# Performance work log

Measured on AMD Instinct MI355X. Metric: run time of the kernel, lower is better.

Reference implementation:

```python
import jax, jax.numpy as jnp
import numpy as np

B, T, IN, H, OUT = 512, 2048, 16, 128, 8


def setup_inputs() -> dict:
    key = jax.random.key(0)
    ks = jax.random.split(key, 12)
    s = 0.05
    return {
        "x": jax.random.normal(ks[0], (B, T, IN), dtype=jnp.float32),
        "W_ih0": jax.random.normal(ks[1], (3 * H, IN), dtype=jnp.float32) * s,
        "W_hh0": jax.random.normal(ks[2], (3 * H, H), dtype=jnp.float32) * s,
        "b_ih0": jax.random.normal(ks[3], (3 * H,), dtype=jnp.float32) * s,
        "b_hh0": jax.random.normal(ks[4], (3 * H,), dtype=jnp.float32) * s,
        "W_ih1": jax.random.normal(ks[5], (3 * H, H), dtype=jnp.float32) * s,
        "W_hh1": jax.random.normal(ks[6], (3 * H, H), dtype=jnp.float32) * s,
        "b_ih1": jax.random.normal(ks[7], (3 * H,), dtype=jnp.float32) * s,
        "b_hh1": jax.random.normal(ks[8], (3 * H,), dtype=jnp.float32) * s,
        "W_out": jax.random.normal(ks[9], (OUT, H), dtype=jnp.float32) * s,
        "b_out": jax.random.normal(ks[10], (OUT,), dtype=jnp.float32) * s,
    }


def _gru_cell(xg, h, W_hh, b_hh):
    # xg: precomputed x @ W_ih.T + b_ih, shape [B, 3H]; PyTorch gate order r,z,n
    hg = h @ W_hh.T + b_hh
    xr, xz, xn = jnp.split(xg, 3, axis=-1)
    hr, hz, hn = jnp.split(hg, 3, axis=-1)
    r = jax.nn.sigmoid(xr + hr)
    z = jax.nn.sigmoid(xz + hz)
    n = jnp.tanh(xn + r * hn)
    return (1.0 - z) * n + z * h


def reference(x, W_ih0, W_hh0, b_ih0, b_hh0, W_ih1, W_hh1, b_ih1, b_hh1, W_out, b_out):
    # Precompute layer-0 input gates for all timesteps: [T, B, 3H]
    xg0 = jnp.einsum('bti,gi->tbg', x, W_ih0) + b_ih0

    def step(carry, xg_t):
        h0, h1 = carry
        h0 = _gru_cell(xg_t, h0, W_hh0, b_hh0)
        xg1 = h0 @ W_ih1.T + b_ih1
        h1 = _gru_cell(xg1, h1, W_hh1, b_hh1)
        return (h0, h1), h1

    h0 = jnp.zeros((x.shape[0], W_hh0.shape[1]), dtype=x.dtype)
    h1 = jnp.zeros((x.shape[0], W_hh1.shape[1]), dtype=x.dtype)
    _, h1_seq = jax.lax.scan(step, (h0, h1), xg0)  # [T, B, H]
    out = jnp.einsum('tbh,oh->bto', h1_seq, W_out) + b_out  # [B, T, OUT]
    return out
```

## Files before the change

kernel.cpp:

```cpp
#include <hip/hip_runtime.h>


typedef unsigned int  uint;
typedef unsigned short ushort;
typedef _Float16 v8h __attribute__((ext_vector_type(8)));
typedef float    v4f __attribute__((ext_vector_type(4)));
typedef uint     v2u __attribute__((ext_vector_type(2)));

#define Tq   2048
#define INq  16
#define Hq   128
#define OUTq 8
#define BW   16

#define MFMA(a,b,c) __builtin_amdgcn_mfma_f32_16x16x32_f16((a),(b),(c),0,0,0)
#define BAR() do { asm volatile("s_waitcnt lgkmcnt(0)" ::: "memory"); \
                   __builtin_amdgcn_s_barrier(); \
                   asm volatile("" ::: "memory"); } while(0)

__device__ __forceinline__ float sigm(float x){
  return __builtin_amdgcn_rcpf(1.0f + __expf(-x));
}
__device__ __forceinline__ float tanh_f(float x){
  return 1.0f - 2.0f*__builtin_amdgcn_rcpf(__expf(2.0f*x) + 1.0f);
}
__device__ __forceinline__ uint packh2(float lo, float hi){
  _Float16 a=(_Float16)lo, b=(_Float16)hi;
  return (uint)__builtin_bit_cast(ushort,a) | ((uint)__builtin_bit_cast(ushort,b)<<16);
}
__device__ __forceinline__ v4f ld4(const float* p){
  return *reinterpret_cast<const v4f*>(p);
}

__global__ __launch_bounds__(512,2) void gru2_kernel(
    const float* __restrict__ x,
    const float* __restrict__ Wih0, const float* __restrict__ Whh0,
    const float* __restrict__ bih0, const float* __restrict__ bhh0,
    const float* __restrict__ Wih1, const float* __restrict__ Whh1,
    const float* __restrict__ bih1, const float* __restrict__ bhh1,
    const float* __restrict__ Wout, const float* __restrict__ bout,
    float* __restrict__ out)
{
  const int tid  = threadIdx.x;
  const int lane = tid & 63;
  const int w    = tid >> 6;
  const int nb   = lane & 15;
  const int bg   = lane >> 4;
  const int b0   = blockIdx.x * BW;
  const int hb   = 16*w + nb;

  __shared__ __align__(16) _Float16 hA0[2][2048];
  __shared__ __align__(16) _Float16 hA1[2][2048];
  for (int i=tid; i<2048; i+=512){ ((uint*)hA0)[i]=0u; ((uint*)hA1)[i]=0u; }

  const float* xrow = x + (size_t)(b0+nb)*Tq*INq;
  float4 xfa, xfb;
  if (bg < 2){
    xfa = *(const float4*)(xrow + 0*INq + bg*8);
    xfb = *(const float4*)(xrow + 0*INq + bg*8 + 4);
  }

  v8h Fhh0[3][4], Fih1[3][4], Fhh1[3][4], Fx[3], Fo[4];
  #pragma unroll
  for (int g=0; g<3; ++g){
    const int r = g*Hq + hb;
    #pragma unroll
    for (int ks=0; ks<4; ++ks){
      const float* p0 = &Whh0[r*Hq + ks*32 + bg*8];
      const float* p1 = &Wih1[r*Hq + ks*32 + bg*8];
      const float* p2 = &Whh1[r*Hq + ks*32 + bg*8];
      v8h a, b, c;
      #pragma unroll
      for (int e=0;e<8;++e){ a[e]=(_Float16)p0[e]; b[e]=(_Float16)p1[e]; c[e]=(_Float16)p2[e]; }
      Fhh0[g][ks]=a; Fih1[g][ks]=b; Fhh1[g][ks]=c;
    }
    v8h vx;
    #pragma unroll
    for (int e=0;e<8;++e) vx[e]=(_Float16)0.f;
    if (bg < 2){
      const float* p = &Wih0[r*INq + bg*8];
      #pragma unroll
      for (int e=0;e<8;++e) vx[e]=(_Float16)p[e];
    }
    Fx[g]=vx;
  }
  #pragma unroll
  for (int ks=0; ks<4; ++ks){
    v8h v;
    #pragma unroll
    for (int e=0;e<8;++e) v[e]=(_Float16)0.f;
    if (nb < OUTq){
      const float* p = &Wout[nb*Hq + ks*32 + bg*8];
      #pragma unroll
      for (int e=0;e<8;++e) v[e]=(_Float16)p[e];
    }
    Fo[ks]=v;
  }

  const int hb4 = 16*w + bg*4;
  const v4f bR4  = ld4(bih0+hb4)      + ld4(bhh0+hb4);
  const v4f bZ4  = ld4(bih0+Hq+hb4)   + ld4(bhh0+Hq+hb4);
  const v4f bNX4 = ld4(bih0+2*Hq+hb4);
  const v4f bNH4 = ld4(bhh0+2*Hq+hb4);
  const v4f cR4  = ld4(bih1+hb4)      + ld4(bhh1+hb4);
  const v4f cZ4  = ld4(bih1+Hq+hb4)   + ld4(bhh1+Hq+hb4);
  const v4f cNX4 = ld4(bih1+2*Hq+hb4);
  const v4f cNH4 = ld4(bhh1+2*Hq+hb4);
  v4f bo4 = {0.f,0.f,0.f,0.f};
  if (bg < 2) bo4 = ld4(bout + bg*4);

  float h0s[4] = {0,0,0,0};
  float h1s[4] = {0,0,0,0};

  int rb[4];
  #pragma unroll
  for (int ks=0; ks<4; ++ks) rb[ks] = nb*128 + (((ks*4+bg) ^ nb))*8;
  const int wof = nb*128 + (((2*w + (bg>>1)) ^ nb))*8 + (bg&1)*4;

  __syncthreads();

  for (int t=0; t<Tq; ++t){
    const int cur = t&1, prv = cur^1;

    v8h ax;
    #pragma unroll
    for (int e=0;e<8;++e) ax[e]=(_Float16)0.f;
    if (bg < 2){
      ax[0]=(_Float16)xfa.x; ax[1]=(_Float16)xfa.y; ax[2]=(_Float16)xfa.z; ax[3]=(_Float16)xfa.w;
      ax[4]=(_Float16)xfb.x; ax[5]=(_Float16)xfb.y; ax[6]=(_Float16)xfb.z; ax[7]=(_Float16)xfb.w;
    }

    v4f aR=bR4, aZ=bZ4, aNX=bNX4, aNH=bNH4;
    aR  = MFMA(Fx[0], ax, aR);
    aZ  = MFMA(Fx[1], ax, aZ);
    aNX = MFMA(Fx[2], ax, aNX);
    if (bg < 2){
      const int tn = (t+1 < Tq) ? t+1 : Tq-1;
      xfa = *(const float4*)(xrow + tn*INq + bg*8);
      xfb = *(const float4*)(xrow + tn*INq + bg*8 + 4);
    }
    #pragma unroll
    for (int ks=0; ks<4; ++ks){
      v8h a = *(const v8h*)&hA0[prv][rb[ks]];
      aR  = MFMA(Fhh0[0][ks], a, aR);
      aZ  = MFMA(Fhh0[1][ks], a, aZ);
      aNH = MFMA(Fhh0[2][ks], a, aNH);
    }
    float hn0[4];
    #pragma unroll
    for (int j=0;j<4;++j){
      float r = sigm(aR[j]);
      float z = sigm(aZ[j]);
      float n = tanh_f(aNX[j] + r*aNH[j]);
      float h = n + z*(h0s[j]-n);
      h0s[j]=h; hn0[j]=h;
    }
    { v2u pk; pk[0]=packh2(hn0[0],hn0[1]); pk[1]=packh2(hn0[2],hn0[3]);
      *(v2u*)&hA0[cur][wof] = pk; }
    BAR();

    v4f cR=cR4, cZ=cZ4, cNX=cNX4, cNH=cNH4;
    #pragma unroll
    for (int ks=0; ks<4; ++ks){
      v8h a0 = *(const v8h*)&hA0[cur][rb[ks]];
      v8h a1 = *(const v8h*)&hA1[prv][rb[ks]];
      cR  = MFMA(Fih1[0][ks], a0, cR);
      cZ  = MFMA(Fih1[1][ks], a0, cZ);
      cNX = MFMA(Fih1[2][ks], a0, cNX);
      cR  = MFMA(Fhh1[0][ks], a1, cR);
      cZ  = MFMA(Fhh1[1][ks], a1, cZ);
      cNH = MFMA(Fhh1[2][ks], a1, cNH);
    }
    if (w == 7){
      v4f oac = {0.f,0.f,0.f,0.f};
      #pragma unroll
      for (int ks=0; ks<4; ++ks){
        v8h a1 = *(const v8h*)&hA1[prv][rb[ks]];
        oac = MFMA(Fo[ks], a1, oac);
      }
      if (t > 0 && bg < 2){
        float4 o;
        o.x=oac[0]+bo4[0]; o.y=oac[1]+bo4[1]; o.z=oac[2]+bo4[2]; o.w=oac[3]+bo4[3];
        *(float4*)&out[((size_t)(b0+nb)*Tq + (t-1))*OUTq + bg*4] = o;
      }
    }
    float hn1[4];
    #pragma unroll
    for (int j=0;j<4;++j){
      float r = sigm(cR[j]);
      float z = sigm(cZ[j]);
      float n = tanh_f(cNX[j] + r*cNH[j]);
      float h = n + z*(h1s[j]-n);
      h1s[j]=h; hn1[j]=h;
    }
    { v2u pk; pk[0]=packh2(hn1[0],hn1[1]); pk[1]=packh2(hn1[2],hn1[3]);
      *(v2u*)&hA1[cur][wof] = pk; }
    BAR();
  }

  if (w == 7){
    v4f oac = {0.f,0.f,0.f,0.f};
    #pragma unroll
    for (int ks=0; ks<4; ++ks){
      v8h a1 = *(const v8h*)&hA1[1][rb[ks]];
      oac = MFMA(Fo[ks], a1, oac);
    }
    if (bg < 2){
      float4 o;
      o.x=oac[0]+bo4[0]; o.y=oac[1]+bo4[1]; o.z=oac[2]+bo4[2]; o.w=oac[3]+bo4[3];
      *(float4*)&out[((size_t)(b0+nb)*Tq + (Tq-1))*OUTq + bg*4] = o;
    }
  }
}

extern "C" void kernel_launch(void* const* d_in, const int* in_sizes, int n_in,
                              void* d_out, int out_size, void* d_ws, size_t ws_size,
                              hipStream_t stream) {
  const float* x    = (const float*)d_in[0];
  const float* Wih0 = (const float*)d_in[1];
  const float* Whh0 = (const float*)d_in[2];
  const float* bih0 = (const float*)d_in[3];
  const float* bhh0 = (const float*)d_in[4];
  const float* Wih1 = (const float*)d_in[5];
  const float* Whh1 = (const float*)d_in[6];
  const float* bih1 = (const float*)d_in[7];
  const float* bhh1 = (const float*)d_in[8];
  const float* Wout = (const float*)d_in[9];
  const float* bo   = (const float*)d_in[10];
  gru2_kernel<<<dim3(32), dim3(512), 0, stream>>>(
      x, Wih0, Whh0, bih0, bhh0, Wih1, Whh1, bih1, bhh1, Wout, bo,
      (float*)d_out);
}
```

Baseline: 3.296 ms.

## Skew layer-1 by one timestep to use one barrier per step

Restructures the recurrence so that each tick computes layer 0 for step t and layer 1 for step t-1 together, both reading only state from the previous tick. This halves the block-wide barriers per timestep and lets the MFMA chains for the two layers interleave. Biases move to shared memory to free registers, and the x prefetch is deepened to two steps with a manual unroll by two. The cost is an extra drain tick and more complex buffer indexing, plus possible register pressure from holding both layers' fragments at once.

```diff
diff --git a/kernel.cpp b/kernel.cpp
--- a/kernel.cpp
+++ b/kernel.cpp
@@ -27,9 +27,6 @@
 __device__ __forceinline__ uint packh2(float lo, float hi){
   _Float16 a=(_Float16)lo, b=(_Float16)hi;
   return (uint)__builtin_bit_cast(ushort,a) | ((uint)__builtin_bit_cast(ushort,b)<<16);
-}
-__device__ __forceinline__ v4f ld4(const float* p){
-  return *reinterpret_cast<const v4f*>(p);
 }
 
 __global__ __launch_bounds__(512,2) void gru2_kernel(
@@ -48,16 +45,32 @@
   const int bg   = lane >> 4;
   const int b0   = blockIdx.x * BW;
   const int hb   = 16*w + nb;
+  const int hb4  = 16*w + bg*4;
 
   __shared__ __align__(16) _Float16 hA0[2][2048];
   __shared__ __align__(16) _Float16 hA1[2][2048];
+  __shared__ __align__(16) float    bl[1024];
   for (int i=tid; i<2048; i+=512){ ((uint*)hA0)[i]=0u; ((uint*)hA1)[i]=0u; }
+  for (int i=tid; i<1024; i+=512){
+    const int k=i>>7, h=i&127; float v;
+    if      (k==0) v = bih0[h]       + bhh0[h];
+    else if (k==1) v = bih0[128+h]   + bhh0[128+h];
+    else if (k==2) v = bih0[256+h];
+    else if (k==3) v = bhh0[256+h];
+    else if (k==4) v = bih1[h]       + bhh1[h];
+    else if (k==5) v = bih1[128+h]   + bhh1[128+h];
+    else if (k==6) v = bih1[256+h];
+    else           v = bhh1[256+h];
+    bl[i]=v;
+  }
 
   const float* xrow = x + (size_t)(b0+nb)*Tq*INq;
-  float4 xfa, xfb;
+  float4 xqa[2], xqb[2];
   if (bg < 2){
-    xfa = *(const float4*)(xrow + 0*INq + bg*8);
-    xfb = *(const float4*)(xrow + 0*INq + bg*8 + 4);
+    xqa[0]=*(const float4*)(xrow + 0*INq + bg*8);
+    xqb[0]=*(const float4*)(xrow + 0*INq + bg*8 + 4);
+    xqa[1]=*(const float4*)(xrow + 1*INq + bg*8);
+    xqb[1]=*(const float4*)(xrow + 1*INq + bg*8 + 4);
   }
 
   v8h Fhh0[3][4], Fih1[3][4], Fhh1[3][4], Fx[3], Fo[4];
@@ -96,107 +109,114 @@
     }
     Fo[ks]=v;
   }
-
-  const int hb4 = 16*w + bg*4;
-  const v4f bR4  = ld4(bih0+hb4)      + ld4(bhh0+hb4);
-  const v4f bZ4  = ld4(bih0+Hq+hb4)   + ld4(bhh0+Hq+hb4);
-  const v4f bNX4 = ld4(bih0+2*Hq+hb4);
-  const v4f bNH4 = ld4(bhh0+2*Hq+hb4);
-  const v4f cR4  = ld4(bih1+hb4)      + ld4(bhh1+hb4);
-  const v4f cZ4  = ld4(bih1+Hq+hb4)   + ld4(bhh1+Hq+hb4);
-  const v4f cNX4 = ld4(bih1+2*Hq+hb4);
-  const v4f cNH4 = ld4(bhh1+2*Hq+hb4);
   v4f bo4 = {0.f,0.f,0.f,0.f};
-  if (bg < 2) bo4 = ld4(bout + bg*4);
+  if (bg < 2) bo4 = *(const v4f*)(bout + bg*4);
 
   float h0s[4] = {0,0,0,0};
   float h1s[4] = {0,0,0,0};
 
   int rb[4];
   #pragma unroll
-  for (int ks=0; ks<4; ++ks) rb[ks] = nb*128 + (((ks*4+bg) ^ nb))*8;
+  for (int ks=0; ks<4; ++ks) rb[ks] = nb*128 + ((ks*4+bg) ^ nb)*8;
   const int wof = nb*128 + (((2*w + (bg>>1)) ^ nb))*8 + (bg&1)*4;
 
   __syncthreads();
 
-  for (int t=0; t<Tq; ++t){
-    const int cur = t&1, prv = cur^1;
-
-    v8h ax;
-    #pragma unroll
-    for (int e=0;e<8;++e) ax[e]=(_Float16)0.f;
-    if (bg < 2){
-      ax[0]=(_Float16)xfa.x; ax[1]=(_Float16)xfa.y; ax[2]=(_Float16)xfa.z; ax[3]=(_Float16)xfa.w;
-      ax[4]=(_Float16)xfb.x; ax[5]=(_Float16)xfb.y; ax[6]=(_Float16)xfb.z; ax[7]=(_Float16)xfb.w;
-    }
-
-    v4f aR=bR4, aZ=bZ4, aNX=bNX4, aNH=bNH4;
-    aR  = MFMA(Fx[0], ax, aR);
-    aZ  = MFMA(Fx[1], ax, aZ);
-    aNX = MFMA(Fx[2], ax, aNX);
-    if (bg < 2){
-      const int tn = (t+1 < Tq) ? t+1 : Tq-1;
-      xfa = *(const float4*)(xrow + tn*INq + bg*8);
-      xfb = *(const float4*)(xrow + tn*INq + bg*8 + 4);
-    }
-    #pragma unroll
-    for (int ks=0; ks<4; ++ks){
-      v8h a = *(const v8h*)&hA0[prv][rb[ks]];
-      aR  = MFMA(Fhh0[0][ks], a, aR);
-      aZ  = MFMA(Fhh0[1][ks], a, aZ);
-      aNH = MFMA(Fhh0[2][ks], a, aNH);
-    }
-    float hn0[4];
-    #pragma unroll
-    for (int j=0;j<4;++j){
-      float r = sigm(aR[j]);
-      float z = sigm(aZ[j]);
-      float n = tanh_f(aNX[j] + r*aNH[j]);
-      float h = n + z*(h0s[j]-n);
-      h0s[j]=h; hn0[j]=h;
-    }
-    { v2u pk; pk[0]=packh2(hn0[0],hn0[1]); pk[1]=packh2(hn0[2],hn0[3]);
-      *(v2u*)&hA0[cur][wof] = pk; }
-    BAR();
-
-    v4f cR=cR4, cZ=cZ4, cNX=cNX4, cNH=cNH4;
-    #pragma unroll
-    for (int ks=0; ks<4; ++ks){
-      v8h a0 = *(const v8h*)&hA0[cur][rb[ks]];
-      v8h a1 = *(const v8h*)&hA1[prv][rb[ks]];
-      cR  = MFMA(Fih1[0][ks], a0, cR);
-      cZ  = MFMA(Fih1[1][ks], a0, cZ);
-      cNX = MFMA(Fih1[2][ks], a0, cNX);
-      cR  = MFMA(Fhh1[0][ks], a1, cR);
-      cZ  = MFMA(Fhh1[1][ks], a1, cZ);
-      cNH = MFMA(Fhh1[2][ks], a1, cNH);
-    }
-    if (w == 7){
-      v4f oac = {0.f,0.f,0.f,0.f};
-      #pragma unroll
-      for (int ks=0; ks<4; ++ks){
-        v8h a1 = *(const v8h*)&hA1[prv][rb[ks]];
-        oac = MFMA(Fo[ks], a1, oac);
-      }
-      if (t > 0 && bg < 2){
-        float4 o;
-        o.x=oac[0]+bo4[0]; o.y=oac[1]+bo4[1]; o.z=oac[2]+bo4[2]; o.w=oac[3]+bo4[3];
-        *(float4*)&out[((size_t)(b0+nb)*Tq + (t-1))*OUTq + bg*4] = o;
-      }
-    }
-    float hn1[4];
-    #pragma unroll
-    for (int j=0;j<4;++j){
-      float r = sigm(cR[j]);
-      float z = sigm(cZ[j]);
-      float n = tanh_f(cNX[j] + r*cNH[j]);
-      float h = n + z*(h1s[j]-n);
-      h1s[j]=h; hn1[j]=h;
-    }
-    { v2u pk; pk[0]=packh2(hn1[0],hn1[1]); pk[1]=packh2(hn1[2],hn1[3]);
-      *(v2u*)&hA1[cur][wof] = pk; }
-    BAR();
-  }
+#define TICK(T_, CUR, DOH0) do {                                            \
+  const int t_ = (T_);                                                      \
+  v4f aR  = *(const v4f*)&bl[0*128+hb4];                                    \
+  v4f aZ  = *(const v4f*)&bl[1*128+hb4];                                    \
+  v4f aNX = *(const v4f*)&bl[2*128+hb4];                                    \
+  v4f aNH = *(const v4f*)&bl[3*128+hb4];                                    \
+  v4f cR  = *(const v4f*)&bl[4*128+hb4];                                    \
+  v4f cZ  = *(const v4f*)&bl[5*128+hb4];                                    \
+  v4f cNX = *(const v4f*)&bl[6*128+hb4];                                    \
+  v4f cNH = *(const v4f*)&bl[7*128+hb4];                                    \
+  v8h a0[4], a1[4];                                                         \
+  _Pragma("unroll")                                                         \
+  for (int ks=0; ks<4; ++ks){                                               \
+    a0[ks] = *(const v8h*)&hA0[(CUR)^1][rb[ks]];                            \
+    a1[ks] = *(const v8h*)&hA1[(CUR)][rb[ks]];                              \
+  }                                                                         \
+  v8h ax;                                                                   \
+  _Pragma("unroll")                                                         \
+  for (int e=0;e<8;++e) ax[e]=(_Float16)0.f;                                \
+  if (bg < 2){                                                              \
+    ax[0]=(_Float16)xqa[CUR].x; ax[1]=(_Float16)xqa[CUR].y;                 \
+    ax[2]=(_Float16)xqa[CUR].z; ax[3]=(_Float16)xqa[CUR].w;                 \
+    ax[4]=(_Float16)xqb[CUR].x; ax[5]=(_Float16)xqb[CUR].y;                 \
+    ax[6]=(_Float16)xqb[CUR].z; ax[7]=(_Float16)xqb[CUR].w;                 \
+    int tn = t_ + 2; if (tn > Tq-1) tn = Tq-1;                              \
+    xqa[CUR]=*(const float4*)(xrow + tn*INq + bg*8);                        \
+    xqb[CUR]=*(const float4*)(xrow + tn*INq + bg*8 + 4);                    \
+  }                                                                         \
+  if (DOH0){                                                                \
+    aR  = MFMA(Fx[0], ax, aR);                                              \
+    aZ  = MFMA(Fx[1], ax, aZ);                                              \
+    aNX = MFMA(Fx[2], ax, aNX);                                             \
+    _Pragma("unroll")                                                       \
+    for (int ks=0; ks<4; ++ks){                                             \
+      aR  = MFMA(Fhh0[0][ks], a0[ks], aR);                                  \
+      aZ  = MFMA(Fhh0[1][ks], a0[ks], aZ);                                  \
+      aNH = MFMA(Fhh0[2][ks], a0[ks], aNH);                                 \
+    }                                                                       \
+  }                                                                         \
+  if (t_ > 0){                                                              \
+    _Pragma("unroll")                                                       \
+    for (int ks=0; ks<4; ++ks){                                             \
+      cR  = MFMA(Fih1[0][ks], a0[ks], cR);                                  \
+      cZ  = MFMA(Fih1[1][ks], a0[ks], cZ);                                  \
+      cNX = MFMA(Fih1[2][ks], a0[ks], cNX);                                 \
+      cR  = MFMA(Fhh1[0][ks], a1[ks], cR);                                  \
+      cZ  = MFMA(Fhh1[1][ks], a1[ks], cZ);                                  \
+      cNH = MFMA(Fhh1[2][ks], a1[ks], cNH);                                 \
+    }                                                                       \
+  }                                                                         \
+  if (DOH0){                                                                \
+    float hn0[4];                                                           \
+    _Pragma("unroll")                                                       \
+    for (int j=0;j<4;++j){                                                  \
+      float r = sigm(aR[j]);                                                \
+      float z = sigm(aZ[j]);                                                \
+      float n = tanh_f(aNX[j] + r*aNH[j]);                                  \
+      float h = n + z*(h0s[j]-n);                                           \
+      h0s[j]=h; hn0[j]=h;                                                   \
+    }                                                                       \
+    v2u pk; pk[0]=packh2(hn0[0],hn0[1]); pk[1]=packh2(hn0[2],hn0[3]);       \
+    *(v2u*)&hA0[(CUR)][wof] = pk;                                           \
+  }                                                                         \
+  if (t_ > 0){                                                              \
+    if (w == 7){                                                            \
+      v4f oac = {0.f,0.f,0.f,0.f};                                          \
+      _Pragma("unroll")                                                     \
+      for (int ks=0; ks<4; ++ks) oac = MFMA(Fo[ks], a1[ks], oac);           \
+      if (t_ >= 2 && bg < 2){                                               \
+        float4 o;                                                           \
+        o.x=oac[0]+bo4[0]; o.y=oac[1]+bo4[1];                               \
+        o.z=oac[2]+bo4[2]; o.w=oac[3]+bo4[3];                               \
+        *(float4*)&out[((size_t)(b0+nb)*Tq + (t_-2))*OUTq + bg*4] = o;      \
+      }                                                                     \
+    }                                                                       \
+    float hn1[4];                                                           \
+    _Pragma("unroll")                                                       \
+    for (int j=0;j<4;++j){                                                  \
+      float r = sigm(cR[j]);                                                \
+      float z = sigm(cZ[j]);                                                \
+      float n = tanh_f(cNX[j] + r*cNH[j]);                                  \
+      float h = n + z*(h1s[j]-n);                                           \
+      h1s[j]=h; hn1[j]=h;                                                   \
+    }                                                                       \
+    v2u pk; pk[0]=packh2(hn1[0],hn1[1]); pk[1]=packh2(hn1[2],hn1[3]);       \
+    *(v2u*)&hA1[(CUR)^1][wof] = pk;                                         \
+  }                                                                         \
+  BAR();                                                                    \
+} while(0)
+
+  for (int t2=0; t2<Tq; t2+=2){
+    TICK(t2,   0, true);
+    TICK(t2+1, 1, true);
+  }
+  TICK(Tq, 0, false);
 
   if (w == 7){
     v4f oac = {0.f,0.f,0.f,0.f};
```

Measured after the change: 5.048 ms. 53.2% more time.

## Skew GRU layers by one timestep to drop a barrier per step

Applied to the files above, without the earlier changes.

The second GRU layer now runs one timestep behind the first inside the same loop iteration. Both layers consume the same h0(t-1) fragments loaded once from LDS, which cuts the per-step block barriers from two to one. Explicit prologue and epilogue iterations handle the skew, and the hA1 double-buffer indexing is flipped to match. Gate biases move from registers into an LDS table, which lowers register pressure at the cost of extra LDS reads each step. The output projection MFMA now runs in every wave, adding redundant matrix work to avoid a divergent branch.

```diff
diff --git a/kernel.cpp b/kernel.cpp
--- a/kernel.cpp
+++ b/kernel.cpp
@@ -27,9 +27,6 @@
 __device__ __forceinline__ uint packh2(float lo, float hi){
   _Float16 a=(_Float16)lo, b=(_Float16)hi;
   return (uint)__builtin_bit_cast(ushort,a) | ((uint)__builtin_bit_cast(ushort,b)<<16);
-}
-__device__ __forceinline__ v4f ld4(const float* p){
-  return *reinterpret_cast<const v4f*>(p);
 }
 
 __global__ __launch_bounds__(512,2) void gru2_kernel(
@@ -48,10 +45,24 @@
   const int bg   = lane >> 4;
   const int b0   = blockIdx.x * BW;
   const int hb   = 16*w + nb;
+  const int hb4  = 16*w + bg*4;
 
   __shared__ __align__(16) _Float16 hA0[2][2048];
   __shared__ __align__(16) _Float16 hA1[2][2048];
+  __shared__ __align__(16) float    bl[1024];
   for (int i=tid; i<2048; i+=512){ ((uint*)hA0)[i]=0u; ((uint*)hA1)[i]=0u; }
+  for (int i=tid; i<1024; i+=512){
+    const int k=i>>7, h=i&127; float v;
+    if      (k==0) v = bih0[h]       + bhh0[h];
+    else if (k==1) v = bih0[128+h]   + bhh0[128+h];
+    else if (k==2) v = bih0[256+h];
+    else if (k==3) v = bhh0[256+h];
+    else if (k==4) v = bih1[h]       + bhh1[h];
+    else if (k==5) v = bih1[128+h]   + bhh1[128+h];
+    else if (k==6) v = bih1[256+h];
+    else           v = bhh1[256+h];
+    bl[i]=v;
+  }
 
   const float* xrow = x + (size_t)(b0+nb)*Tq*INq;
   float4 xfa, xfb;
@@ -96,55 +107,80 @@
     }
     Fo[ks]=v;
   }
-
-  const int hb4 = 16*w + bg*4;
-  const v4f bR4  = ld4(bih0+hb4)      + ld4(bhh0+hb4);
-  const v4f bZ4  = ld4(bih0+Hq+hb4)   + ld4(bhh0+Hq+hb4);
-  const v4f bNX4 = ld4(bih0+2*Hq+hb4);
-  const v4f bNH4 = ld4(bhh0+2*Hq+hb4);
-  const v4f cR4  = ld4(bih1+hb4)      + ld4(bhh1+hb4);
-  const v4f cZ4  = ld4(bih1+Hq+hb4)   + ld4(bhh1+Hq+hb4);
-  const v4f cNX4 = ld4(bih1+2*Hq+hb4);
-  const v4f cNH4 = ld4(bhh1+2*Hq+hb4);
   v4f bo4 = {0.f,0.f,0.f,0.f};
-  if (bg < 2) bo4 = ld4(bout + bg*4);
+  if (bg < 2) bo4 = *(const v4f*)(bout + bg*4);
 
   float h0s[4] = {0,0,0,0};
   float h1s[4] = {0,0,0,0};
 
   int rb[4];
   #pragma unroll
-  for (int ks=0; ks<4; ++ks) rb[ks] = nb*128 + (((ks*4+bg) ^ nb))*8;
+  for (int ks=0; ks<4; ++ks) rb[ks] = nb*128 + ((ks*4+bg) ^ nb)*8;
   const int wof = nb*128 + (((2*w + (bg>>1)) ^ nb))*8 + (bg&1)*4;
 
   __syncthreads();
 
-  for (int t=0; t<Tq; ++t){
-    const int cur = t&1, prv = cur^1;
-
+  {
+    v4f aR  = *(const v4f*)&bl[0*128+hb4];
+    v4f aZ  = *(const v4f*)&bl[1*128+hb4];
+    v4f aNX = *(const v4f*)&bl[2*128+hb4];
+    v4f aNH = *(const v4f*)&bl[3*128+hb4];
     v8h ax;
     #pragma unroll
     for (int e=0;e<8;++e) ax[e]=(_Float16)0.f;
     if (bg < 2){
       ax[0]=(_Float16)xfa.x; ax[1]=(_Float16)xfa.y; ax[2]=(_Float16)xfa.z; ax[3]=(_Float16)xfa.w;
       ax[4]=(_Float16)xfb.x; ax[5]=(_Float16)xfb.y; ax[6]=(_Float16)xfb.z; ax[7]=(_Float16)xfb.w;
-    }
-
-    v4f aR=bR4, aZ=bZ4, aNX=bNX4, aNH=bNH4;
+      xfa = *(const float4*)(xrow + 1*INq + bg*8);
+      xfb = *(const float4*)(xrow + 1*INq + bg*8 + 4);
+    }
     aR  = MFMA(Fx[0], ax, aR);
     aZ  = MFMA(Fx[1], ax, aZ);
     aNX = MFMA(Fx[2], ax, aNX);
+    float hn0[4];
+    #pragma unroll
+    for (int j=0;j<4;++j){
+      float r = sigm(aR[j]);
+      float z = sigm(aZ[j]);
+      float n = tanh_f(aNX[j] + r*aNH[j]);
+      float h = n - z*n;
+      h0s[j]=h; hn0[j]=h;
+    }
+    v2u pk; pk[0]=packh2(hn0[0],hn0[1]); pk[1]=packh2(hn0[2],hn0[3]);
+    *(v2u*)&hA0[0][wof] = pk;
+    BAR();
+  }
+
+  for (int t=1; t<Tq; ++t){
+    const int cur = t&1, prv = cur^1;
+
+    v8h a0k[4];
+    #pragma unroll
+    for (int ks=0; ks<4; ++ks) a0k[ks] = *(const v8h*)&hA0[prv][rb[ks]];
+    v4f aR  = *(const v4f*)&bl[0*128+hb4];
+    v4f aZ  = *(const v4f*)&bl[1*128+hb4];
+    v4f aNX = *(const v4f*)&bl[2*128+hb4];
+    v4f aNH = *(const v4f*)&bl[3*128+hb4];
+
+    v8h ax;
+    #pragma unroll
+    for (int e=0;e<8;++e) ax[e]=(_Float16)0.f;
     if (bg < 2){
-      const int tn = (t+1 < Tq) ? t+1 : Tq-1;
+      ax[0]=(_Float16)xfa.x; ax[1]=(_Float16)xfa.y; ax[2]=(_Float16)xfa.z; ax[3]=(_Float16)xfa.w;
+      ax[4]=(_Float16)xfb.x; ax[5]=(_Float16)xfb.y; ax[6]=(_Float16)xfb.z; ax[7]=(_Float16)xfb.w;
+      int tn = t+1; if (tn > Tq-1) tn = Tq-1;
       xfa = *(const float4*)(xrow + tn*INq + bg*8);
       xfb = *(const float4*)(xrow + tn*INq + bg*8 + 4);
     }
-    #pragma unroll
-    for (int ks=0; ks<4; ++ks){
-      v8h a = *(const v8h*)&hA0[prv][rb[ks]];
-      aR  = MFMA(Fhh0[0][ks], a, aR);
-      aZ  = MFMA(Fhh0[1][ks], a, aZ);
-      aNH = MFMA(Fhh0[2][ks], a, aNH);
+
+    aR  = MFMA(Fx[0], ax, aR);
+    aZ  = MFMA(Fx[1], ax, aZ);
+    aNX = MFMA(Fx[2], ax, aNX);
+    #pragma unroll
+    for (int ks=0; ks<4; ++ks){
+      aR  = MFMA(Fhh0[0][ks], a0k[ks], aR);
+      aZ  = MFMA(Fhh0[1][ks], a0k[ks], aZ);
+      aNH = MFMA(Fhh0[2][ks], a0k[ks], aNH);
     }
     float hn0[4];
     #pragma unroll
@@ -157,32 +193,22 @@
     }
     { v2u pk; pk[0]=packh2(hn0[0],hn0[1]); pk[1]=packh2(hn0[2],hn0[3]);
       *(v2u*)&hA0[cur][wof] = pk; }
-    BAR();
-
-    v4f cR=cR4, cZ=cZ4, cNX=cNX4, cNH=cNH4;
-    #pragma unroll
-    for (int ks=0; ks<4; ++ks){
-      v8h a0 = *(const v8h*)&hA0[cur][rb[ks]];
-      v8h a1 = *(const v8h*)&hA1[prv][rb[ks]];
-      cR  = MFMA(Fih1[0][ks], a0, cR);
-      cZ  = MFMA(Fih1[1][ks], a0, cZ);
-      cNX = MFMA(Fih1[2][ks], a0, cNX);
+
+    v4f cR  = *(const v4f*)&bl[4*128+hb4];
+    v4f cZ  = *(const v4f*)&bl[5*128+hb4];
+    v4f cNX = *(const v4f*)&bl[6*128+hb4];
+    v4f cNH = *(const v4f*)&bl[7*128+hb4];
+    v4f oac = {0.f,0.f,0.f,0.f};
+    #pragma unroll
+    for (int ks=0; ks<4; ++ks){
+      v8h a1 = *(const v8h*)&hA1[cur][rb[ks]];
+      cR  = MFMA(Fih1[0][ks], a0k[ks], cR);
+      cZ  = MFMA(Fih1[1][ks], a0k[ks], cZ);
+      cNX = MFMA(Fih1[2][ks], a0k[ks], cNX);
       cR  = MFMA(Fhh1[0][ks], a1, cR);
       cZ  = MFMA(Fhh1[1][ks], a1, cZ);
       cNH = MFMA(Fhh1[2][ks], a1, cNH);
-    }
-    if (w == 7){
-      v4f oac = {0.f,0.f,0.f,0.f};
-      #pragma unroll
-      for (int ks=0; ks<4; ++ks){
-        v8h a1 = *(const v8h*)&hA1[prv][rb[ks]];
-        oac = MFMA(Fo[ks], a1, oac);
-      }
-      if (t > 0 && bg < 2){
-        float4 o;
-        o.x=oac[0]+bo4[0]; o.y=oac[1]+bo4[1]; o.z=oac[2]+bo4[2]; o.w=oac[3]+bo4[3];
-        *(float4*)&out[((size_t)(b0+nb)*Tq + (t-1))*OUTq + bg*4] = o;
-      }
+      oac = MFMA(Fo[ks],      a1, oac);
     }
     float hn1[4];
     #pragma unroll
@@ -194,7 +220,53 @@
       h1s[j]=h; hn1[j]=h;
     }
     { v2u pk; pk[0]=packh2(hn1[0],hn1[1]); pk[1]=packh2(hn1[2],hn1[3]);
-      *(v2u*)&hA1[cur][wof] = pk; }
+      *(v2u*)&hA1[prv][wof] = pk; }
+
+    if (w == 7 && bg < 2){
+      int to = t-2; if (to < 0) to = 0;
+      float4 o;
+      o.x=oac[0]+bo4[0]; o.y=oac[1]+bo4[1]; o.z=oac[2]+bo4[2]; o.w=oac[3]+bo4[3];
+      *(float4*)&out[((size_t)(b0+nb)*Tq + to)*OUTq + bg*4] = o;
+    }
+    BAR();
+  }
+
+  {
+    v8h a0k[4];
+    #pragma unroll
+    for (int ks=0; ks<4; ++ks) a0k[ks] = *(const v8h*)&hA0[1][rb[ks]];
+    v4f cR  = *(const v4f*)&bl[4*128+hb4];
+    v4f cZ  = *(const v4f*)&bl[5*128+hb4];
+    v4f cNX = *(const v4f*)&bl[6*128+hb4];
+    v4f cNH = *(const v4f*)&bl[7*128+hb4];
+    v4f oac = {0.f,0.f,0.f,0.f};
+    #pragma unroll
+    for (int ks=0; ks<4; ++ks){
+      v8h a1 = *(const v8h*)&hA1[0][rb[ks]];
+      cR  = MFMA(Fih1[0][ks], a0k[ks], cR);
+      cZ  = MFMA(Fih1[1][ks], a0k[ks], cZ);
+      cNX = MFMA(Fih1[2][ks], a0k[ks], cNX);
+      cR  = MFMA(Fhh1[0][ks], a1, cR);
+      cZ  = MFMA(Fhh1[1][ks], a1, cZ);
+      cNH = MFMA(Fhh1[2][ks], a1, cNH);
+      oac = MFMA(Fo[ks],      a1, oac);
+    }
+    float hn1[4];
+    #pragma unroll
+    for (int j=0;j<4;++j){
+      float r = sigm(cR[j]);
+      float z = sigm(cZ[j]);
+      float n = tanh_f(cNX[j] + r*cNH[j]);
+      float h = n + z*(h1s[j]-n);
+      h1s[j]=h; hn1[j]=h;
+    }
+    { v2u pk; pk[0]=packh2(hn1[0],hn1[1]); pk[1]=packh2(hn1[2],hn1[3]);
+      *(v2u*)&hA1[1][wof] = pk; }
+    if (w == 7 && bg < 2){
+      float4 o;
+      o.x=oac[0]+bo4[0]; o.y=oac[1]+bo4[1]; o.z=oac[2]+bo4[2]; o.w=oac[3]+bo4[3];
+      *(float4*)&out[((size_t)(b0+nb)*Tq + (Tq-2))*OUTq + bg*4] = o;
+    }
     BAR();
   }
 
```

Result: slower. 3.378 ms (+2.5%).

## Split waves into layer-0 and layer-1 groups pipelined across timesteps

Applied to the files above, without the earlier changes.

Waves 0-3 now compute layer 0 for step t while waves 4-7 compute layer 1 for step t-1 at the same time. This wavefront pipeline needs one barrier per step instead of two, and each wave holds weights for only one layer, covering 32 hidden units. Biases move to shared memory to free registers, and the output projection runs on wave 3 with two steps of lag. In exchange the loop runs one extra iteration, the two wave groups do unequal work, and more MFMAs run serially per wave.

```diff
diff --git a/kernel.cpp b/kernel.cpp
--- a/kernel.cpp
+++ b/kernel.cpp
@@ -11,7 +11,6 @@
 #define INq  16
 #define Hq   128
 #define OUTq 8
-#define BW   16
 
 #define MFMA(a,b,c) __builtin_amdgcn_mfma_f32_16x16x32_f16((a),(b),(c),0,0,0)
 #define BAR() do { asm volatile("s_waitcnt lgkmcnt(0)" ::: "memory"); \
@@ -27,9 +26,6 @@
 __device__ __forceinline__ uint packh2(float lo, float hi){
   _Float16 a=(_Float16)lo, b=(_Float16)hi;
   return (uint)__builtin_bit_cast(ushort,a) | ((uint)__builtin_bit_cast(ushort,b)<<16);
-}
-__device__ __forceinline__ v4f ld4(const float* p){
-  return *reinterpret_cast<const v4f*>(p);
 }
 
 __global__ __launch_bounds__(512,2) void gru2_kernel(
@@ -44,166 +40,206 @@
   const int tid  = threadIdx.x;
   const int lane = tid & 63;
   const int w    = tid >> 6;
+  const int wl   = w & 3;
+  const bool isL0 = (w < 4);
   const int nb   = lane & 15;
   const int bg   = lane >> 4;
-  const int b0   = blockIdx.x * BW;
-  const int hb   = 16*w + nb;
+  const int b0   = blockIdx.x * 16;
 
   __shared__ __align__(16) _Float16 hA0[2][2048];
   __shared__ __align__(16) _Float16 hA1[2][2048];
+  __shared__ __align__(16) float    bl[1024];
   for (int i=tid; i<2048; i+=512){ ((uint*)hA0)[i]=0u; ((uint*)hA1)[i]=0u; }
+  for (int i=tid; i<1024; i+=512){
+    const int k=i>>7, h=i&127; float v;
+    if      (k==0) v = bih0[h]       + bhh0[h];
+    else if (k==1) v = bih0[128+h]   + bhh0[128+h];
+    else if (k==2) v = bih0[256+h];
+    else if (k==3) v = bhh0[256+h];
+    else if (k==4) v = bih1[h]       + bhh1[h];
+    else if (k==5) v = bih1[128+h]   + bhh1[128+h];
+    else if (k==6) v = bih1[256+h];
+    else           v = bhh1[256+h];
+    bl[i]=v;
+  }
 
   const float* xrow = x + (size_t)(b0+nb)*Tq*INq;
   float4 xfa, xfb;
-  if (bg < 2){
-    xfa = *(const float4*)(xrow + 0*INq + bg*8);
-    xfb = *(const float4*)(xrow + 0*INq + bg*8 + 4);
-  }
-
-  v8h Fhh0[3][4], Fih1[3][4], Fhh1[3][4], Fx[3], Fo[4];
+  if (isL0 && bg < 2){
+    xfa = *(const float4*)(xrow + bg*8);
+    xfb = *(const float4*)(xrow + bg*8 + 4);
+  }
+
+  v8h W1[2][3][4], W2[2][3][4], W3[4];
   #pragma unroll
-  for (int g=0; g<3; ++g){
-    const int r = g*Hq + hb;
+  for (int ta=0; ta<2; ++ta){
+    const int R = 32*wl + 16*ta + nb;
+    #pragma unroll
+    for (int g=0; g<3; ++g){
+      const int r = g*Hq + R;
+      #pragma unroll
+      for (int ks=0; ks<4; ++ks){
+        const float* p1 = isL0 ? &Whh0[r*Hq + ks*32 + bg*8]
+                               : &Wih1[r*Hq + ks*32 + bg*8];
+        v8h a;
+        #pragma unroll
+        for (int e=0;e<8;++e) a[e]=(_Float16)p1[e];
+        W1[ta][g][ks]=a;
+      }
+      if (isL0){
+        v8h vx;
+        #pragma unroll
+        for (int e=0;e<8;++e) vx[e]=(_Float16)0.f;
+        if (bg < 2){
+          const float* p = &Wih0[r*INq + bg*8];
+          #pragma unroll
+          for (int e=0;e<8;++e) vx[e]=(_Float16)p[e];
+        }
+        W2[ta][g][0]=vx;
+      } else {
+        #pragma unroll
+        for (int ks=0; ks<4; ++ks){
+          const float* p2 = &Whh1[r*Hq + ks*32 + bg*8];
+          v8h c;
+          #pragma unroll
+          for (int e=0;e<8;++e) c[e]=(_Float16)p2[e];
+          W2[ta][ks==0?g:g][ks]=c;
+        }
+      }
+    }
+  }
+  if (w == 3){
     #pragma unroll
     for (int ks=0; ks<4; ++ks){
-      const float* p0 = &Whh0[r*Hq + ks*32 + bg*8];
-      const float* p1 = &Wih1[r*Hq + ks*32 + bg*8];
-      const float* p2 = &Whh1[r*Hq + ks*32 + bg*8];
-      v8h a, b, c;
-      #pragma unroll
-      for (int e=0;e<8;++e){ a[e]=(_Float16)p0[e]; b[e]=(_Float16)p1[e]; c[e]=(_Float16)p2[e]; }
-      Fhh0[g][ks]=a; Fih1[g][ks]=b; Fhh1[g][ks]=c;
-    }
-    v8h vx;
-    #pragma unroll
-    for (int e=0;e<8;++e) vx[e]=(_Float16)0.f;
-    if (bg < 2){
-      const float* p = &Wih0[r*INq + bg*8];
-      #pragma unroll
-      for (int e=0;e<8;++e) vx[e]=(_Float16)p[e];
-    }
-    Fx[g]=vx;
-  }
-  #pragma unroll
-  for (int ks=0; ks<4; ++ks){
-    v8h v;
-    #pragma unroll
-    for (int e=0;e<8;++e) v[e]=(_Float16)0.f;
-    if (nb < OUTq){
-      const float* p = &Wout[nb*Hq + ks*32 + bg*8];
-      #pragma unroll
-      for (int e=0;e<8;++e) v[e]=(_Float16)p[e];
-    }
-    Fo[ks]=v;
-  }
-
-  const int hb4 = 16*w + bg*4;
-  const v4f bR4  = ld4(bih0+hb4)      + ld4(bhh0+hb4);
-  const v4f bZ4  = ld4(bih0+Hq+hb4)   + ld4(bhh0+Hq+hb4);
-  const v4f bNX4 = ld4(bih0+2*Hq+hb4);
-  const v4f bNH4 = ld4(bhh0+2*Hq+hb4);
-  const v4f cR4  = ld4(bih1+hb4)      + ld4(bhh1+hb4);
-  const v4f cZ4  = ld4(bih1+Hq+hb4)   + ld4(bhh1+Hq+hb4);
-  const v4f cNX4 = ld4(bih1+2*Hq+hb4);
-  const v4f cNH4 = ld4(bhh1+2*Hq+hb4);
+      v8h v;
+      #pragma unroll
+      for (int e=0;e<8;++e) v[e]=(_Float16)0.f;
+      if (nb < OUTq){
+        const float* p = &Wout[nb*Hq + ks*32 + bg*8];
+        #pragma unroll
+        for (int e=0;e<8;++e) v[e]=(_Float16)p[e];
+      }
+      W3[ks]=v;
+    }
+  }
   v4f bo4 = {0.f,0.f,0.f,0.f};
-  if (bg < 2) bo4 = ld4(bout + bg*4);
-
-  float h0s[4] = {0,0,0,0};
-  float h1s[4] = {0,0,0,0};
+  if (bg < 2) bo4 = *(const v4f*)(bout + bg*4);
+  const v4f zf = {0.f,0.f,0.f,0.f};
+
+  float hs[2][4] = {{0,0,0,0},{0,0,0,0}};
 
   int rb[4];
   #pragma unroll
-  for (int ks=0; ks<4; ++ks) rb[ks] = nb*128 + (((ks*4+bg) ^ nb))*8;
-  const int wof = nb*128 + (((2*w + (bg>>1)) ^ nb))*8 + (bg&1)*4;
+  for (int ks=0; ks<4; ++ks) rb[ks] = nb*128 + ((ks*4+bg) ^ nb)*8;
+  const int wof0 = nb*128 + (((4*wl + 0 + (bg>>1)) ^ nb))*8 + (bg&1)*4;
+  const int wof1 = nb*128 + (((4*wl + 2 + (bg>>1)) ^ nb))*8 + (bg&1)*4;
 
   __syncthreads();
 
-  for (int t=0; t<Tq; ++t){
-    const int cur = t&1, prv = cur^1;
-
-    v8h ax;
-    #pragma unroll
-    for (int e=0;e<8;++e) ax[e]=(_Float16)0.f;
-    if (bg < 2){
-      ax[0]=(_Float16)xfa.x; ax[1]=(_Float16)xfa.y; ax[2]=(_Float16)xfa.z; ax[3]=(_Float16)xfa.w;
-      ax[4]=(_Float16)xfb.x; ax[5]=(_Float16)xfb.y; ax[6]=(_Float16)xfb.z; ax[7]=(_Float16)xfb.w;
-    }
-
-    v4f aR=bR4, aZ=bZ4, aNX=bNX4, aNH=bNH4;
-    aR  = MFMA(Fx[0], ax, aR);
-    aZ  = MFMA(Fx[1], ax, aZ);
-    aNX = MFMA(Fx[2], ax, aNX);
-    if (bg < 2){
-      const int tn = (t+1 < Tq) ? t+1 : Tq-1;
-      xfa = *(const float4*)(xrow + tn*INq + bg*8);
-      xfb = *(const float4*)(xrow + tn*INq + bg*8 + 4);
-    }
-    #pragma unroll
-    for (int ks=0; ks<4; ++ks){
-      v8h a = *(const v8h*)&hA0[prv][rb[ks]];
-      aR  = MFMA(Fhh0[0][ks], a, aR);
-      aZ  = MFMA(Fhh0[1][ks], a, aZ);
-      aNH = MFMA(Fhh0[2][ks], a, aNH);
-    }
-    float hn0[4];
-    #pragma unroll
-    for (int j=0;j<4;++j){
-      float r = sigm(aR[j]);
-      float z = sigm(aZ[j]);
-      float n = tanh_f(aNX[j] + r*aNH[j]);
-      float h = n + z*(h0s[j]-n);
-      h0s[j]=h; hn0[j]=h;
-    }
-    { v2u pk; pk[0]=packh2(hn0[0],hn0[1]); pk[1]=packh2(hn0[2],hn0[3]);
-      *(v2u*)&hA0[cur][wof] = pk; }
+  for (int t=0; t<=Tq; ++t){
+    const int pb = (t+1)&1;
+    const int cb = t&1;
+
+    if (isL0){
+      if (t < Tq){
+        v8h ax;
+        #pragma unroll
+        for (int e=0;e<8;++e) ax[e]=(_Float16)0.f;
+        if (bg < 2){
+          ax[0]=(_Float16)xfa.x; ax[1]=(_Float16)xfa.y; ax[2]=(_Float16)xfa.z; ax[3]=(_Float16)xfa.w;
+          ax[4]=(_Float16)xfb.x; ax[5]=(_Float16)xfb.y; ax[6]=(_Float16)xfb.z; ax[7]=(_Float16)xfb.w;
+          int tn = t+1; if (tn > Tq-1) tn = Tq-1;
+          xfa = *(const float4*)(xrow + tn*INq + bg*8);
+          xfb = *(const float4*)(xrow + tn*INq + bg*8 + 4);
+        }
+        v8h a0k[4];
+        #pragma unroll
+        for (int ks=0; ks<4; ++ks) a0k[ks] = *(const v8h*)&hA0[pb][rb[ks]];
+        #pragma unroll
+        for (int ta=0; ta<2; ++ta){
+          const int hb4 = 32*wl + 16*ta + bg*4;
+          v4f aR  = *(const v4f*)&bl[0*128+hb4];
+          v4f aZ  = *(const v4f*)&bl[1*128+hb4];
+          v4f aNX = *(const v4f*)&bl[2*128+hb4];
+          v4f aNH = *(const v4f*)&bl[3*128+hb4];
+          aR  = MFMA(W2[ta][0][0], ax, aR);
+          aZ  = MFMA(W2[ta][1][0], ax, aZ);
+          aNX = MFMA(W2[ta][2][0], ax, aNX);
+          #pragma unroll
+          for (int ks=0; ks<4; ++ks){
+            aR  = MFMA(W1[ta][0][ks], a0k[ks], aR);
+            aZ  = MFMA(W1[ta][1][ks], a0k[ks], aZ);
+            aNH = MFMA(W1[ta][2][ks], a0k[ks], aNH);
+          }
+          float hn[4];
+          #pragma unroll
+          for (int j=0;j<4;++j){
+            float r = sigm(aR[j]);
+            float z = sigm(aZ[j]);
+            float n = tanh_f(aNX[j] + r*aNH[j]);
+            float h = n + z*(hs[ta][j]-n);
+            hs[ta][j]=h; hn[j]=h;
+          }
+          v2u pk; pk[0]=packh2(hn[0],hn[1]); pk[1]=packh2(hn[2],hn[3]);
+          *(v2u*)&hA0[cb][ta ? wof1 : wof0] = pk;
+        }
+      }
+      if (w == 3 && t >= 1){
+        v4f oac = zf;
+        #pragma unroll
+        for (int ks=0; ks<4; ++ks){
+          v8h a1 = *(const v8h*)&hA1[cb][rb[ks]];
+          oac = MFMA(W3[ks], a1, oac);
+        }
+        if (t >= 2 && bg < 2){
+          float4 o;
+          o.x=oac[0]+bo4[0]; o.y=oac[1]+bo4[1]; o.z=oac[2]+bo4[2]; o.w=oac[3]+bo4[3];
+          *(float4*)&out[((size_t)(b0+nb)*Tq + (t-2))*OUTq + bg*4] = o;
+        }
+      }
+    } else if (t >= 1){
+      v8h a0k[4];
+      #pragma unroll
+      for (int ks=0; ks<4; ++ks) a0k[ks] = *(const v8h*)&hA0[pb][rb[ks]];
+      #pragma unroll
+      for (int ta=0; ta<2; ++ta){
+        const int hb4 = 32*wl + 16*ta + bg*4;
+        v4f cR  = *(const v4f*)&bl[4*128+hb4];
+        v4f cZ  = *(const v4f*)&bl[5*128+hb4];
+        v4f cNX = *(const v4f*)&bl[6*128+hb4];
+        v4f cNH = *(const v4f*)&bl[7*128+hb4];
+        #pragma unroll
+        for (int ks=0; ks<4; ++ks){
+          v8h a1 = *(const v8h*)&hA1[cb][rb[ks]];
+          cR  = MFMA(W1[ta][0][ks], a0k[ks], cR);
+          cZ  = MFMA(W1[ta][1][ks], a0k[ks], cZ);
+          cNX = MFMA(W1[ta][2][ks], a0k[ks], cNX);
+          cR  = MFMA(W2[ta][0][ks], a1, cR);
+          cZ  = MFMA(W2[ta][1][ks], a1, cZ);
+          cNH = MFMA(W2[ta][2][ks], a1, cNH);
+        }
+        float hn[4];
+        #pragma unroll
+        for (int j=0;j<4;++j){
+          float r = sigm(cR[j]);
+          float z = sigm(cZ[j]);
+          float n = tanh_f(cNX[j] + r*cNH[j]);
+          float h = n + z*(hs[ta][j]-n);
+          hs[ta][j]=h; hn[j]=h;
+        }
+        v2u pk; pk[0]=packh2(hn[0],hn[1]); pk[1]=packh2(hn[2],hn[3]);
+        *(v2u*)&hA1[pb][ta ? wof1 : wof0] = pk;
+      }
+    }
     BAR();
-
-    v4f cR=cR4, cZ=cZ4, cNX=cNX4, cNH=cNH4;
-    #pragma unroll
-    for (int ks=0; ks<4; ++ks){
-      v8h a0 = *(const v8h*)&hA0[cur][rb[ks]];
-      v8h a1 = *(const v8h*)&hA1[prv][rb[ks]];
-      cR  = MFMA(Fih1[0][ks], a0, cR);
-      cZ  = MFMA(Fih1[1][ks], a0, cZ);
-      cNX = MFMA(Fih1[2][ks], a0, cNX);
-      cR  = MFMA(Fhh1[0][ks], a1, cR);
-      cZ  = MFMA(Fhh1[1][ks], a1, cZ);
-      cNH = MFMA(Fhh1[2][ks], a1, cNH);
-    }
-    if (w == 7){
-      v4f oac = {0.f,0.f,0.f,0.f};
-      #pragma unroll
-      for (int ks=0; ks<4; ++ks){
-        v8h a1 = *(const v8h*)&hA1[prv][rb[ks]];
-        oac = MFMA(Fo[ks], a1, oac);
-      }
-      if (t > 0 && bg < 2){
-        float4 o;
-        o.x=oac[0]+bo4[0]; o.y=oac[1]+bo4[1]; o.z=oac[2]+bo4[2]; o.w=oac[3]+bo4[3];
-        *(float4*)&out[((size_t)(b0+nb)*Tq + (t-1))*OUTq + bg*4] = o;
-      }
-    }
-    float hn1[4];
-    #pragma unroll
-    for (int j=0;j<4;++j){
-      float r = sigm(cR[j]);
-      float z = sigm(cZ[j]);
-      float n = tanh_f(cNX[j] + r*cNH[j]);
-      float h = n + z*(h1s[j]-n);
-      h1s[j]=h; hn1[j]=h;
-    }
-    { v2u pk; pk[0]=packh2(hn1[0],hn1[1]); pk[1]=packh2(hn1[2],hn1[3]);
-      *(v2u*)&hA1[cur][wof] = pk; }
-    BAR();
-  }
-
-  if (w == 7){
-    v4f oac = {0.f,0.f,0.f,0.f};
+  }
+
+  if (w == 3){
+    v4f oac = zf;
     #pragma unroll
     for (int ks=0; ks<4; ++ks){
       v8h a1 = *(const v8h*)&hA1[1][rb[ks]];
-      oac = MFMA(Fo[ks], a1, oac);
+      oac = MFMA(W3[ks], a1, oac);
     }
     if (bg < 2){
       float4 o;
```

Result: slower. 3.488 ms (+5.8%).
